# Optimization experiments

Hardware: AMD Instinct MI355X
Metric: run time of the kernel (lower is better)

Reference implementation:

```python
import jax, jax.numpy as jnp
import numpy as np

INPUT_DIM = 64
OUTPUT_DIM = 128
KNN = 10          # hardcoded min(10, N) in source
RADIUS = 0.02     # density radius in source


def setup_inputs() -> dict:
    key = jax.random.key(0)
    k1, k2, k3, k4, k5, k6, k7 = jax.random.split(key, 7)
    B, N = 2, 8192
    points = jax.random.uniform(k1, (B, N, 3), dtype=jnp.float32)
    features = jax.random.normal(k2, (B, N, INPUT_DIM), dtype=jnp.float32)
    leaf_mask = jax.random.randint(k3, (B, N), 0, 2) > 0
    d_in = INPUT_DIM + 6
    s1 = 1.0 / np.sqrt(d_in)
    s2 = 1.0 / np.sqrt(OUTPUT_DIM)
    W1 = jax.random.uniform(k4, (d_in, OUTPUT_DIM), jnp.float32, -s1, s1)
    b1 = jax.random.uniform(k5, (OUTPUT_DIM,), jnp.float32, -s1, s1)
    W2 = jax.random.uniform(k6, (OUTPUT_DIM, OUTPUT_DIM), jnp.float32, -s2, s2)
    b2 = jax.random.uniform(k7, (OUTPUT_DIM,), jnp.float32, -s2, s2)
    return {"points": points, "features": features, "leaf_mask": leaf_mask,
            "W1": W1, "b1": b1, "W2": W2, "b2": b2}


def _leaf_geometry(points, mask):
    # points: [N,3], mask: [N] bool -> [N,6]
    mask_f = mask.astype(points.dtype)
    cnt = jnp.maximum(mask_f.sum(), 1.0)
    center = (points * mask_f[:, None]).sum(0) / cnt      # mean of masked points
    rel = points - center                                  # [N,3]
    dist_c = jnp.linalg.norm(rel, axis=1)                  # dist to leaf center
    rel_h = rel[:, 2]                                      # relative height
    horiz = jnp.linalg.norm(rel[:, :2], axis=1)            # horizontal distance
    # pairwise euclidean distances [N,N]; used only for thresholding and knn
    sq = jnp.sum(points * points, axis=1)
    d2 = sq[:, None] + sq[None, :] - 2.0 * (points @ points.T)
    dist = jax.lax.stop_gradient(jnp.sqrt(jnp.maximum(d2, 0.0)))
    density = jnp.sum((dist < RADIUS) & mask[None, :], axis=1).astype(points.dtype)
    # KNN (smallest distances, includes self) -> local PCA curvature
    _, idx = jax.lax.top_k(-dist, KNN)                     # [N,KNN]
    neighbors = points[idx]                                # [N,KNN,3]
    centered = neighbors - points[:, None, :]
    cov = jnp.einsum('nki,nkj->nij', centered, centered) / float(KNN)  # [N,3,3]
    ev = jnp.linalg.eigh(cov)[0]                           # ascending eigenvalues
    curv = ev[:, 0] / (ev[:, 2] + 1e-8)
    rad = jnp.arctan2(rel[:, 1], rel[:, 0])
    geom = jnp.stack([dist_c, rel_h, horiz, density, curv, rad], axis=1)
    # source returns zeros when mask is empty
    return jnp.where(mask_f.sum() > 0, geom, jnp.zeros_like(geom))


def reference(points, features, leaf_mask, W1, b1, W2, b2):
    geom = jax.vmap(_leaf_geometry)(points, leaf_mask)     # [B,N,6]
    combined = jnp.concatenate([features, geom], axis=-1)  # [B,N,input_dim+6]
    h = jax.nn.relu(combined @ W1 + b1)
    return jax.nn.relu(h @ W2 + b2)                        # [B,N,output_dim]
```

## Files before the change

kernel.cpp:

```cpp
#include <hip/hip_runtime.h>
#include <math.h>
#include <stdint.h>

#define B_SZ   2
#define N_PTS  8192
#define IN_DIM 64
#define D_IN   70
#define ODIM   128
#define NQ_ALL (B_SZ * N_PTS)
#define RADIUS_F 0.02f

#define GDIM  32
#define NCELL (GDIM * GDIM * GDIM)
#define HCELL 0.03125f

#define SUP     4
#define NSUP_AX 8
#define NSUPER  (NSUP_AX * NSUP_AX * NSUP_AX)
#define SCAP    352
#define LCAP    24
#define MAXROWS 100

typedef unsigned long long u64;

__device__ __forceinline__ void insert11(u64 (&best)[11], u64 key) {
#pragma unroll
  for (int j = 10; j >= 1; --j) {
    u64 hi = (best[j - 1] > key) ? best[j - 1] : key;
    best[j] = (best[j] < hi) ? best[j] : hi;
  }
  best[0] = (best[0] < key) ? best[0] : key;
}
__device__ __forceinline__ void insert10(u64 (&best)[10], u64 key) {
#pragma unroll
  for (int j = 9; j >= 1; --j) {
    u64 hi = (best[j - 1] > key) ? best[j - 1] : key;
    best[j] = (best[j] < hi) ? best[j] : hi;
  }
  best[0] = (best[0] < key) ? best[0] : key;
}

__device__ __forceinline__ float sq3(float x, float y, float z) {
  return __fadd_rn(__fadd_rn(__fmul_rn(x, x), __fmul_rn(y, y)), __fmul_rn(z, z));
}

__device__ __forceinline__ int cellOf(float v) {
  int c = (int)(v * 32.0f);
  return min(max(c, 0), GDIM - 1);
}

__device__ __forceinline__ void geom_epilogue(const float* __restrict__ P,
                                              const int (&idxs)[10], float dens,
                                              float px, float py, float pz,
                                              float4 ctr, float* __restrict__ g) {
  double c00 = 0, c01 = 0, c02 = 0, c11 = 0, c12 = 0, c22 = 0;
#pragma unroll
  for (int j = 0; j < 10; ++j) {
    const int idx = idxs[j];
    const float nx = P[3 * idx + 0], ny = P[3 * idx + 1], nz = P[3 * idx + 2];
    const float ex = __fsub_rn(nx, px);
    const float ey = __fsub_rn(ny, py);
    const float ez = __fsub_rn(nz, pz);
    c00 += (double)ex * ex; c01 += (double)ex * ey; c02 += (double)ex * ez;
    c11 += (double)ey * ey; c12 += (double)ey * ez; c22 += (double)ez * ez;
  }
  const double a00 = c00 / 10.0, a01 = c01 / 10.0, a02 = c02 / 10.0;
  const double a11 = c11 / 10.0, a12 = c12 / 10.0, a22 = c22 / 10.0;

  double p1 = a01 * a01 + a02 * a02 + a12 * a12;
  double qq = (a00 + a11 + a22) / 3.0;
  double p2 = (a00 - qq) * (a00 - qq) + (a11 - qq) * (a11 - qq) +
              (a22 - qq) * (a22 - qq) + 2.0 * p1;
  double ev0, ev2;
  if (p2 <= 1e-60) {
    ev0 = ev2 = qq;
  } else {
    double p = sqrt(p2 / 6.0);
    double invp = 1.0 / p;
    double b00 = (a00 - qq) * invp, b11 = (a11 - qq) * invp, b22 = (a22 - qq) * invp;
    double b01 = a01 * invp, b02 = a02 * invp, b12 = a12 * invp;
    double detB = b00 * (b11 * b22 - b12 * b12) - b01 * (b01 * b22 - b12 * b02) +
                  b02 * (b01 * b12 - b11 * b02);
    double r = 0.5 * detB;
    r = fmin(1.0, fmax(-1.0, r));
    double phi = acos(r) / 3.0;
    ev2 = qq + 2.0 * p * cos(phi);
    ev0 = qq + 2.0 * p * cos(phi + 2.0943951023931953);
  }
  const float curv = (float)(ev0 / (ev2 + 1e-08));

  const bool on = ctr.w > 0.0f;
  const float rx = __fsub_rn(px, ctr.x);
  const float ry = __fsub_rn(py, ctr.y);
  const float rz = __fsub_rn(pz, ctr.z);
  const float dist_c = sqrtf(sq3(rx, ry, rz));
  const float horiz  = sqrtf(__fadd_rn(__fmul_rn(rx, rx), __fmul_rn(ry, ry)));
  const float rad    = atan2f(ry, rx);

  g[0] = on ? dist_c : 0.0f;
  g[1] = on ? rz : 0.0f;
  g[2] = on ? horiz : 0.0f;
  g[3] = on ? dens : 0.0f;
  g[4] = on ? curv : 0.0f;
  g[5] = on ? rad : 0.0f;
}

__global__ __launch_bounds__(256) void k_center(const float* __restrict__ points,
                                                const int* __restrict__ mask,
                                                float* __restrict__ centerOut) {
  const int b = blockIdx.x;
  const float* P = points + (size_t)b * N_PTS * 3;
  const int* M = mask + (size_t)b * N_PTS;
  double sx = 0.0, sy = 0.0, sz = 0.0, sc = 0.0;
  for (int i = threadIdx.x; i < N_PTS; i += 256) {
    if (M[i] != 0) {
      sx += (double)P[3 * i + 0];
      sy += (double)P[3 * i + 1];
      sz += (double)P[3 * i + 2];
      sc += 1.0;
    }
  }
  __shared__ double sh[4][256];
  sh[0][threadIdx.x] = sx; sh[1][threadIdx.x] = sy;
  sh[2][threadIdx.x] = sz; sh[3][threadIdx.x] = sc;
  __syncthreads();
  for (int off = 128; off > 0; off >>= 1) {
    if ((int)threadIdx.x < off) {
      sh[0][threadIdx.x] += sh[0][threadIdx.x + off];
      sh[1][threadIdx.x] += sh[1][threadIdx.x + off];
      sh[2][threadIdx.x] += sh[2][threadIdx.x + off];
      sh[3][threadIdx.x] += sh[3][threadIdx.x + off];
    }
    __syncthreads();
  }
  if (threadIdx.x == 0) {
    float cf  = (float)sh[3][0];
    float div = fmaxf(cf, 1.0f);
    centerOut[b * 4 + 0] = (float)sh[0][0] / div;
    centerOut[b * 4 + 1] = (float)sh[1][0] / div;
    centerOut[b * 4 + 2] = (float)sh[2][0] / div;
    centerOut[b * 4 + 3] = (cf > 0.0f) ? 1.0f : 0.0f;
  }
}

__global__ __launch_bounds__(256) void k_grid_count(const float* __restrict__ points,
                                                    int* __restrict__ count) {
  const int t = blockIdx.x * 256 + threadIdx.x;
  const int b = t >> 13;
  const int i = t & (N_PTS - 1);
  const float* P = points + (size_t)b * N_PTS * 3;
  const int cx = cellOf(P[3 * i + 0]);
  const int cy = cellOf(P[3 * i + 1]);
  const int cz = cellOf(P[3 * i + 2]);
  atomicAdd(&count[b * NCELL + (cz * GDIM + cy) * GDIM + cx], 1);
}

__global__ __launch_bounds__(1024) void k_scan(const int* __restrict__ count,
                                               int* __restrict__ start,
                                               int* __restrict__ cur) {
  const int b = blockIdx.x;
  const int t = threadIdx.x;
  int c[32]; int sum = 0;
#pragma unroll
  for (int j = 0; j < 32; ++j) { c[j] = count[b * NCELL + t * 32 + j]; sum += c[j]; }
  __shared__ int s[1024];
  s[t] = sum;
  __syncthreads();
  for (int off = 1; off < 1024; off <<= 1) {
    int v = (t >= off) ? s[t - off] : 0;
    __syncthreads();
    if (t >= off) s[t] += v;
    __syncthreads();
  }
  int excl = (t > 0) ? s[t - 1] : 0;
#pragma unroll
  for (int j = 0; j < 32; ++j) {
    start[b * (NCELL + 1) + t * 32 + j] = excl;
    cur[b * NCELL + t * 32 + j] = excl;
    excl += c[j];
  }
  if (t == 1023) start[b * (NCELL + 1) + NCELL] = excl;
}

__global__ __launch_bounds__(256) void k_scatter(const float* __restrict__ points,
                                                 const int* __restrict__ mask,
                                                 int* __restrict__ cur,
                                                 float4* __restrict__ sorted) {
  const int t = blockIdx.x * 256 + threadIdx.x;
  const int b = t >> 13;
  const int i = t & (N_PTS - 1);
  const float* P = points + (size_t)b * N_PTS * 3;
  const float x = P[3 * i + 0], y = P[3 * i + 1], z = P[3 * i + 2];
  const int cell = (cellOf(z) * GDIM + cellOf(y)) * GDIM + cellOf(x);
  const int pos = atomicAdd(&cur[b * NCELL + cell], 1);
  const unsigned wb = (unsigned)i | ((mask[b * N_PTS + i] != 0) ? 0x80000000u : 0u);
  sorted[(size_t)b * N_PTS + pos] = make_float4(x, y, z, __uint_as_float(wb));
}

__global__ __launch_bounds__(64) void k_collect(const float* __restrict__ points,
                                                const float4* __restrict__ sorted,
                                                const int* __restrict__ start,
                                                const float* __restrict__ center,
                                                float* __restrict__ geom,
                                                int* __restrict__ list,
                                                int* __restrict__ listCnt,
                                                float COLLECT_T, float DENS_T,
                                                float THR_CHECK) {
  const int b  = blockIdx.y;
  const int sc = blockIdx.x;
  const int sx = sc & 7, sy = (sc >> 3) & 7, sz = sc >> 6;
  const int lane = threadIdx.x;

  const int* ST = start + b * (NCELL + 1);
  const float4* SP = sorted + (size_t)b * N_PTS;

  const int x0 = SUP * sx, x1 = SUP * sx + SUP - 1;
  const int y0 = SUP * sy, y1 = SUP * sy + SUP - 1;
  const int z0 = SUP * sz, z1 = SUP * sz + SUP - 1;
  const int hx0 = max(x0 - 3, 0), hx1 = min(x1 + 3, GDIM - 1);
  const int hy0 = max(y0 - 3, 0), hy1 = min(y1 + 3, GDIM - 1);
  const int hz0 = max(z0 - 3, 0), hz1 = min(z1 + 3, GDIM - 1);
  const int yc = hy1 - hy0 + 1;
  const int R  = (hz1 - hz0 + 1) * yc;

  __shared__ int    rs[MAXROWS], rp[MAXROWS + 1];
  __shared__ int    qs_[16], qp_[17];
  __shared__ float4 pts4[SCAP];
  __shared__ u64    lbuf[64 * LCAP];

  {
    int qlen = 0, qst = 0;
    if (lane < 16) {
      const int z = z0 + (lane >> 2), y = y0 + (lane & 3);
      const int base = (z * GDIM + y) * GDIM;
      qst  = ST[base + x0];
      qlen = ST[base + x1 + 1] - qst;
    }
    int inc = qlen;
    for (int off = 1; off < 64; off <<= 1) { int v = __shfl_up(inc, off); if (lane >= off) inc += v; }
    if (lane < 16) { qs_[lane] = qst; qp_[lane] = inc - qlen; }
    if (lane == 63) qp_[16] = inc;
  }
  {
    int len[2] = {0, 0}, st2[2] = {0, 0};
#pragma unroll
    for (int k = 0; k < 2; ++k) {
      const int r = lane * 2 + k;
      if (r < R) {
        const int z = hz0 + r / yc, y = hy0 + r % yc;
        const int base = (z * GDIM + y) * GDIM;
        st2[k] = ST[base + hx0];
        len[k] = ST[base + hx1 + 1] - st2[k];
      }
    }
    int sum = len[0] + len[1];
    int inc = sum;
    for (int off = 1; off < 64; off <<= 1) { int v = __shfl_up(inc, off); if (lane >= off) inc += v; }
    int exc = inc - sum;
#pragma unroll
    for (int k = 0; k < 2; ++k) {
      const int r = lane * 2 + k;
      if (r < R) { rs[r] = st2[k]; rp[r] = exc; }
      exc += len[k];
    }
    if (lane == 63) rp[R] = inc;
  }
  __syncthreads();

  const int C    = rp[R];
  const int qtot = qp_[16];
  if (qtot == 0) return;

  if (C > SCAP) {
    for (int t = lane; t < qtot; t += 64) {
      int lo = 0, hi = 15;
      while (lo < hi) { const int mid = (lo + hi + 1) >> 1; if (qp_[mid] <= t) lo = mid; else hi = mid - 1; }
      const int qglob = qs_[lo] + (t - qp_[lo]);
      const int pos = atomicAdd(listCnt, 1);
      list[pos] = (b << 13) | qglob;
    }
    return;
  }

  for (int i = lane; i < C; i += 64) {
    int lo = 0, hi = R - 1;
    while (lo < hi) { const int mid = (lo + hi + 1) >> 1; if (rp[mid] <= i) lo = mid; else hi = mid - 1; }
    pts4[i] = SP[rs[lo] + (i - rp[lo])];
  }
  __syncthreads();

  const float4 ctr = reinterpret_cast<const float4*>(center)[b];
  const float* P = points + (size_t)b * N_PTS * 3;
  const int sub = lane & 3;
  const int gq  = lane >> 2;

  for (int q0 = 0; q0 < qtot; q0 += 16) {
    const int myq = q0 + gq;
    const bool act = (myq < qtot);
    const int mq = act ? myq : 0;
    int lo = 0, hi = 15;
    while (lo < hi) { const int mid = (lo + hi + 1) >> 1; if (qp_[mid] <= mq) lo = mid; else hi = mid - 1; }
    const int qglob = qs_[lo] + (mq - qp_[lo]);
    const float4 qp4 = SP[qglob];
    const int qidx = (int)(__float_as_uint(qp4.w) & 0x7FFFFFFFu);
    const float px = qp4.x, py = qp4.y, pz = qp4.z;
    const float sqq = sq3(px, py, pz);

    int cnt = 0;
    u64* myb = &lbuf[lane * LCAP];
    for (int j = sub; j < C; j += 4) {
      const float4 tp = pts4[j];
      const float sqc = sq3(tp.x, tp.y, tp.z);
      const float dot = __fmaf_rn(pz, tp.z, __fmaf_rn(py, tp.y, __fmul_rn(px, tp.x)));
      const float d2  = __fsub_rn(__fadd_rn(sqq, sqc), __fmul_rn(2.0f, dot));
      const float d2c = fmaxf(d2, 0.0f);
      if (d2c < COLLECT_T) {
        if (cnt < LCAP) {
          const unsigned wb = __float_as_uint(tp.w);
          myb[cnt] = ((u64)__float_as_uint(d2c) << 32)
                   | (u64)(((wb & 0x7FFFFFFFu) << 1) | (wb >> 31));
        }
        ++cnt;
      }
    }

    u64 best[11];
#pragma unroll
    for (int j = 0; j < 11; ++j) best[j] = ~0ull;
    float dens = 0.0f;
    const int m = min(cnt, LCAP);
    for (int i = 0; i < m; ++i) {
      const u64 e = myb[i];
      if ((e & 1ull) && __uint_as_float((unsigned)(e >> 32)) < DENS_T) dens += 1.0f;
      if (e < best[10]) insert11(best, e);
    }
    int cntg = cnt;
    int over = (cnt > LCAP) ? 1 : 0;
#pragma unroll
    for (int s = 1; s < 4; s <<= 1) {
      dens += __shfl_xor(dens, s);
      cntg += __shfl_xor(cntg, s);
      over |= __shfl_xor(over, s);
      u64 ok[11];
#pragma unroll
      for (int j = 0; j < 11; ++j) ok[j] = __shfl_xor(best[j], s);
#pragma unroll
      for (int j = 0; j < 11; ++j) {
        if (ok[j] < best[10]) insert11(best, ok[j]); else break;
      }
    }

    if (act && sub == 0) {
      const float dist9 = sqrtf(__uint_as_float((unsigned)(best[9] >> 32)));
      bool bad = (over != 0) || (cntg < 10) || !(dist9 < THR_CHECK);
      if (cntg >= 11) {
        const float dist10 = sqrtf(__uint_as_float((unsigned)(best[10] >> 32)));
        bad = bad || (dist10 == dist9);
      }
      if (bad) {
        const int pos = atomicAdd(listCnt, 1);
        list[pos] = (b << 13) | qglob;
      } else {
        int idxs[10];
#pragma unroll
        for (int j = 0; j < 10; ++j) idxs[j] = (int)(((unsigned)best[j]) >> 1);
        geom_epilogue(P, idxs, dens, px, py, pz, ctr,
                      geom + ((size_t)b * N_PTS + qidx) * 6);
      }
    }
  }
}

__global__ __launch_bounds__(64) void k_wavefb(const float* __restrict__ points,
                                               const float4* __restrict__ sorted,
                                               const int* __restrict__ start,
                                               const float* __restrict__ center,
                                               float* __restrict__ geom,
                                               int* __restrict__ flags2,
                                               const int* __restrict__ list,
                                               const int* __restrict__ listCnt) {
  const int lane = threadIdx.x;
  const int n = *listCnt;
  for (int it = blockIdx.x; it < n; it += gridDim.x) {
    const int e = list[it];
    const int b = e >> 13, qs = e & (N_PTS - 1);
    const float4* SP = sorted + (size_t)b * N_PTS;
    const int* ST = start + b * (NCELL + 1);
    const float4 qp = SP[qs];
    const int qidx = (int)(__float_as_uint(qp.w) & 0x7FFFFFFFu);
    const float px = qp.x, py = qp.y, pz = qp.z;
    const float sqq = sq3(px, py, pz);
    const int cx = cellOf(px), cy = cellOf(py), cz = cellOf(pz);
    const int xlo = max(cx - 8, 0), xhi = min(cx + 8, GDIM - 1);
    const int ylo = max(cy - 8, 0), yhi = min(cy + 8, GDIM - 1);
    const int zlo = max(cz - 8, 0), zhi = min(cz + 8, GDIM - 1);
    const int ycw = yhi - ylo + 1;
    const int Rw = (zhi - zlo + 1) * ycw;

    u64 best[10];
#pragma unroll
    for (int j = 0; j < 10; ++j) best[j] = ((u64)0x7F800000u << 32) | 0xFFFFFFFFu;
    float dens = 0.0f;

    for (int r = lane; r < Rw; r += 64) {
      const int z = zlo + r / ycw, y = ylo + r % ycw;
      const int base = (z * GDIM + y) * GDIM;
      const int j0 = ST[base + xlo], j1 = ST[base + xhi + 1];
      for (int j = j0; j < j1; ++j) {
        const float4 tp = SP[j];
        const unsigned wb = __float_as_uint(tp.w);
        const float sqc = sq3(tp.x, tp.y, tp.z);
        const float dot = __fmaf_rn(pz, tp.z, __fmaf_rn(py, tp.y, __fmul_rn(px, tp.x)));
        const float d2  = __fsub_rn(__fadd_rn(sqq, sqc), __fmul_rn(2.0f, dot));
        const float dist = sqrtf(fmaxf(d2, 0.0f));
        if ((dist < RADIUS_F) && (wb & 0x80000000u)) dens += 1.0f;
        const u64 key = ((u64)__float_as_uint(dist) << 32) | (wb & 0x7FFFFFFFu);
        if (key < best[9]) insert10(best, key);
      }
    }
#pragma unroll
    for (int s = 1; s < 64; s <<= 1) {
      dens += __shfl_xor(dens, s);
      u64 ok[10];
#pragma unroll
      for (int j = 0; j < 10; ++j) ok[j] = __shfl_xor(best[j], s);
#pragma unroll
      for (int j = 0; j < 10; ++j) {
        if (ok[j] < best[9]) insert10(best, ok[j]); else break;
      }
    }
    if (lane == 0) {
      const float dist9 = __uint_as_float((unsigned)(best[9] >> 32));
      if (dist9 < 0.2494f) {
        const float4 ctr = reinterpret_cast<const float4*>(center)[b];
        const float* P = points + (size_t)b * N_PTS * 3;
        int idxs[10];
#pragma unroll
        for (int j = 0; j < 10; ++j) idxs[j] = (int)(((unsigned)best[j]) & 0x7FFFFFFFu);
        geom_epilogue(P, idxs, dens, px, py, pz, ctr, geom + ((size_t)b * N_PTS + qidx) * 6);
      } else {
        flags2[b * N_PTS + qs] = 1;
      }
    }
  }
}

__global__ __launch_bounds__(256) void k_fallback(const float* __restrict__ points,
                                                  const float4* __restrict__ sorted,
                                                  const int* __restrict__ start,
                                                  const float* __restrict__ center,
                                                  float* __restrict__ geom,
                                                  const int* __restrict__ flags2) {
  const int b = blockIdx.y;
  const int qs = blockIdx.x * 256 + threadIdx.x;
  if (flags2[b * N_PTS + qs] == 0) return;
  const float4 qp = sorted[(size_t)b * N_PTS + qs];
  const unsigned qw = __float_as_uint(qp.w);
  const int qidx = (int)(qw & 0x7FFFFFFFu);

  const float px = qp.x, py = qp.y, pz = qp.z;
  const float sqq = sq3(px, py, pz);
  const int cx = cellOf(px), cy = cellOf(py), cz = cellOf(pz);

  const int* ST = start + b * (NCELL + 1);
  const float4* SP = sorted + (size_t)b * N_PTS;

  u64 best[10];
#pragma unroll
  for (int j = 0; j < 10; ++j) best[j] = ((u64)0x7F800000u << 32) | 0xFFFFFFFFu;
  float dens = 0.0f;

  for (int rho = 0; rho < GDIM; ++rho) {
    const int zlo = max(cz - rho, 0), zhi = min(cz + rho, GDIM - 1);
    const int ylo = max(cy - rho, 0), yhi = min(cy + rho, GDIM - 1);
    for (int z = zlo; z <= zhi; ++z) {
      const int adz = abs(z - cz);
      for (int y = ylo; y <= yhi; ++y) {
        const int ady = abs(y - cy);
        const int m2 = max(adz, ady);
        int ja, jb;
        int ja2 = 0, jb2 = 0;
        const int rowBase = (z * GDIM + y) * GDIM;
        if (m2 == rho) {
          const int xa = max(cx - rho, 0), xb = min(cx + rho, GDIM - 1);
          ja = ST[rowBase + xa]; jb = ST[rowBase + xb + 1];
        } else {
          ja = jb = 0;
          if (cx - rho >= 0)        { ja = ST[rowBase + cx - rho]; jb = ST[rowBase + cx - rho + 1]; }
          if (cx + rho <= GDIM - 1) { ja2 = ST[rowBase + cx + rho]; jb2 = ST[rowBase + cx + rho + 1]; }
        }
#pragma unroll 1
        for (int pass = 0; pass < 2; ++pass) {
          const int j0 = pass ? ja2 : ja;
          const int j1 = pass ? jb2 : jb;
          for (int j = j0; j < j1; ++j) {
            const float4 tp = SP[j];
            const unsigned wb = __float_as_uint(tp.w);
            const float sqc = sq3(tp.x, tp.y, tp.z);
            const float dot = __fmaf_rn(pz, tp.z, __fmaf_rn(py, tp.y, __fmul_rn(px, tp.x)));
            const float d2  = __fsub_rn(__fadd_rn(sqq, sqc), __fmul_rn(2.0f, dot));
            const float dist = sqrtf(fmaxf(d2, 0.0f));
            if ((dist < RADIUS_F) && (wb & 0x80000000u)) dens += 1.0f;
            const u64 key = ((u64)__float_as_uint(dist) << 32) | (wb & 0x7FFFFFFFu);
            if (key < best[9]) insert10(best, key);
          }
        }
      }
    }
    if (rho >= 1) {
      const float dist9 = __uint_as_float((unsigned)(best[9] >> 32));
      if (dist9 < (float)rho * HCELL * 0.999f) break;
    }
  }

  const float4 ctr = reinterpret_cast<const float4*>(center)[b];
  const float* P = points + (size_t)b * N_PTS * 3;
  int idxs[10];
#pragma unroll
  for (int j = 0; j < 10; ++j) idxs[j] = (int)(((unsigned)best[j]) & 0x7FFFFFFFu);
  geom_epilogue(P, idxs, dens, px, py, pz, ctr, geom + ((size_t)b * N_PTS + qidx) * 6);
}

__global__ __launch_bounds__(256) void k_mlp(const float* __restrict__ features,
                                             const float* __restrict__ geom,
                                             const float* __restrict__ W1,
                                             const float* __restrict__ b1,
                                             const float* __restrict__ W2,
                                             const float* __restrict__ b2,
                                             float* __restrict__ out) {
  __shared__ float A[64][74];
  __shared__ float H[64][130];
  const int tid = threadIdx.x;
  const int row0 = blockIdx.x * 64;

  for (int i = tid; i < 64 * IN_DIM; i += 256) {
    int r = i >> 6, k = i & 63;
    A[r][k] = features[(size_t)(row0 + r) * IN_DIM + k];
  }
  for (int i = tid; i < 64 * 8; i += 256) {
    int r = i >> 3, k = i & 7;
    if (k < 6) A[r][IN_DIM + k] = geom[(size_t)(row0 + r) * 6 + k];
  }
  __syncthreads();

  const int ty = tid >> 4;
  const int tx = tid & 15;

  float acc[4][8];
#pragma unroll
  for (int i = 0; i < 4; ++i)
#pragma unroll
    for (int j = 0; j < 8; ++j) acc[i][j] = 0.0f;

#pragma unroll 2
  for (int k = 0; k < D_IN; ++k) {
    float a[4];
#pragma unroll
    for (int i = 0; i < 4; ++i) a[i] = A[ty * 4 + i][k];
    float4 w0 = *reinterpret_cast<const float4*>(&W1[(size_t)k * ODIM + tx * 8]);
    float4 w1 = *reinterpret_cast<const float4*>(&W1[(size_t)k * ODIM + tx * 8 + 4]);
    float w[8] = {w0.x, w0.y, w0.z, w0.w, w1.x, w1.y, w1.z, w1.w};
#pragma unroll
    for (int i = 0; i < 4; ++i)
#pragma unroll
      for (int j = 0; j < 8; ++j) acc[i][j] = fmaf(a[i], w[j], acc[i][j]);
  }

  {
    float4 bb0 = *reinterpret_cast<const float4*>(&b1[tx * 8]);
    float4 bb1 = *reinterpret_cast<const float4*>(&b1[tx * 8 + 4]);
    float bb[8] = {bb0.x, bb0.y, bb0.z, bb0.w, bb1.x, bb1.y, bb1.z, bb1.w};
#pragma unroll
    for (int i = 0; i < 4; ++i) {
      float4 h0 = make_float4(fmaxf(acc[i][0] + bb[0], 0.f), fmaxf(acc[i][1] + bb[1], 0.f),
                              fmaxf(acc[i][2] + bb[2], 0.f), fmaxf(acc[i][3] + bb[3], 0.f));
      float4 h1 = make_float4(fmaxf(acc[i][4] + bb[4], 0.f), fmaxf(acc[i][5] + bb[5], 0.f),
                              fmaxf(acc[i][6] + bb[6], 0.f), fmaxf(acc[i][7] + bb[7], 0.f));
      *reinterpret_cast<float4*>(&H[ty * 4 + i][tx * 8]) = h0;
      *reinterpret_cast<float4*>(&H[ty * 4 + i][tx * 8 + 4]) = h1;
    }
  }
  __syncthreads();

#pragma unroll
  for (int i = 0; i < 4; ++i)
#pragma unroll
    for (int j = 0; j < 8; ++j) acc[i][j] = 0.0f;

#pragma unroll 2
  for (int k = 0; k < ODIM; ++k) {
    float a[4];
#pragma unroll
    for (int i = 0; i < 4; ++i) a[i] = H[ty * 4 + i][k];
    float4 w0 = *reinterpret_cast<const float4*>(&W2[(size_t)k * ODIM + tx * 8]);
    float4 w1 = *reinterpret_cast<const float4*>(&W2[(size_t)k * ODIM + tx * 8 + 4]);
    float w[8] = {w0.x, w0.y, w0.z, w0.w, w1.x, w1.y, w1.z, w1.w};
#pragma unroll
    for (int i = 0; i < 4; ++i)
#pragma unroll
      for (int j = 0; j < 8; ++j) acc[i][j] = fmaf(a[i], w[j], acc[i][j]);
  }

  {
    float4 bb0 = *reinterpret_cast<const float4*>(&b2[tx * 8]);
    float4 bb1 = *reinterpret_cast<const float4*>(&b2[tx * 8 + 4]);
    float bb[8] = {bb0.x, bb0.y, bb0.z, bb0.w, bb1.x, bb1.y, bb1.z, bb1.w};
#pragma unroll
    for (int i = 0; i < 4; ++i) {
      size_t row = (size_t)(row0 + ty * 4 + i);
      float4 o0 = make_float4(fmaxf(acc[i][0] + bb[0], 0.f), fmaxf(acc[i][1] + bb[1], 0.f),
                              fmaxf(acc[i][2] + bb[2], 0.f), fmaxf(acc[i][3] + bb[3], 0.f));
      float4 o1 = make_float4(fmaxf(acc[i][4] + bb[4], 0.f), fmaxf(acc[i][5] + bb[5], 0.f),
                              fmaxf(acc[i][6] + bb[6], 0.f), fmaxf(acc[i][7] + bb[7], 0.f));
      *reinterpret_cast<float4*>(&out[row * ODIM + tx * 8]) = o0;
      *reinterpret_cast<float4*>(&out[row * ODIM + tx * 8 + 4]) = o1;
    }
  }
}

extern "C" void kernel_launch(void* const* d_in, const int* in_sizes, int n_in,
                              void* d_out, int out_size, void* d_ws, size_t ws_size,
                              hipStream_t stream) {
  const float* points   = (const float*)d_in[0];
  const float* features = (const float*)d_in[1];
  const int*   mask     = (const int*)d_in[2];
  const float* W1       = (const float*)d_in[3];
  const float* b1       = (const float*)d_in[4];
  const float* W2       = (const float*)d_in[5];
  const float* b2       = (const float*)d_in[6];
  float* out = (float*)d_out;

  const double Rd   = (double)0.02f;
  const double midd = Rd - ldexp(1.0, -30);
  const double Td   = midd * midd;
  float densT = (float)Td;
  if ((double)densT <= Td) densT = nextafterf(densT, 1.0f);
  const float collectT = 0.0935f * 0.0935f;
  const float thrCheck = 0.0934f;

  char* w = (char*)d_ws;
  size_t off = 0;
  auto take = [&](size_t bytes) { char* p = w + off; off = (off + bytes + 255) & ~(size_t)255; return p; };
  float*  geomBuf   = (float*)take((size_t)NQ_ALL * 6 * 4);
  float*  centerBuf = (float*)take(2 * 16);
  char*   zero0     = (char*)take(0);
  int*    countBuf  = (int*)take((size_t)B_SZ * NCELL * 4);
  int*    flags2Buf = (int*)take((size_t)NQ_ALL * 4);
  int*    listCnt   = (int*)take(4);
  char*   zero1     = (char*)take(0);
  int*    startBuf  = (int*)take((size_t)B_SZ * (NCELL + 1) * 4);
  int*    curBuf    = (int*)take((size_t)B_SZ * NCELL * 4);
  float4* sortedBuf = (float4*)take((size_t)B_SZ * N_PTS * 16);
  int*    listBuf   = (int*)take((size_t)NQ_ALL * 4);
  (void)ws_size;

  hipMemsetAsync(zero0, 0, (size_t)(zero1 - zero0), stream);
  k_center<<<B_SZ, 256, 0, stream>>>(points, mask, centerBuf);
  k_grid_count<<<NQ_ALL / 256, 256, 0, stream>>>(points, countBuf);
  k_scan<<<B_SZ, 1024, 0, stream>>>(countBuf, startBuf, curBuf);
  k_scatter<<<NQ_ALL / 256, 256, 0, stream>>>(points, mask, curBuf, sortedBuf);
  k_collect<<<dim3(NSUPER, B_SZ), 64, 0, stream>>>(points, sortedBuf, startBuf, centerBuf,
                                                   geomBuf, listBuf, listCnt,
                                                   collectT, densT, thrCheck);
  k_wavefb<<<1024, 64, 0, stream>>>(points, sortedBuf, startBuf, centerBuf,
                                    geomBuf, flags2Buf, listBuf, listCnt);
  k_fallback<<<dim3(N_PTS / 256, B_SZ), 256, 0, stream>>>(points, sortedBuf, startBuf,
                                                          centerBuf, geomBuf, flags2Buf);
  k_mlp<<<NQ_ALL / 64, 256, 0, stream>>>(features, geomBuf, W1, b1, W2, b2, out);
}
```

Baseline: 227.2 us.

## Fuse center reduction into grid count, widen collect blocks, shrink MLP row tiles

Folds the mask-center reduction into the grid-count kernel, using wave shuffles and double atomics, and finalizes the center inside the scan kernel, which removes a two-block serial launch. The collect kernel goes from 64 to 128 threads per block, handling 32 queries per pass with a 2x unrolled candidate loop. The MLP uses 32-row tiles so twice as many blocks run with fewer accumulators per thread. Double atomics make the center sum order nondeterministic, and the larger collect blocks use more LDS per block.

```diff
diff --git a/kernel.cpp b/kernel.cpp
--- a/kernel.cpp
+++ b/kernel.cpp
@@ -20,6 +20,8 @@
 #define SCAP    352
 #define LCAP    24
 #define MAXROWS 100
+
+#define MROWS   32
 
 typedef unsigned long long u64;
 
@@ -105,61 +107,52 @@
   g[5] = on ? rad : 0.0f;
 }
 
-__global__ __launch_bounds__(256) void k_center(const float* __restrict__ points,
-                                                const int* __restrict__ mask,
-                                                float* __restrict__ centerOut) {
-  const int b = blockIdx.x;
-  const float* P = points + (size_t)b * N_PTS * 3;
-  const int* M = mask + (size_t)b * N_PTS;
-  double sx = 0.0, sy = 0.0, sz = 0.0, sc = 0.0;
-  for (int i = threadIdx.x; i < N_PTS; i += 256) {
-    if (M[i] != 0) {
-      sx += (double)P[3 * i + 0];
-      sy += (double)P[3 * i + 1];
-      sz += (double)P[3 * i + 2];
-      sc += 1.0;
-    }
-  }
-  __shared__ double sh[4][256];
-  sh[0][threadIdx.x] = sx; sh[1][threadIdx.x] = sy;
-  sh[2][threadIdx.x] = sz; sh[3][threadIdx.x] = sc;
-  __syncthreads();
-  for (int off = 128; off > 0; off >>= 1) {
-    if ((int)threadIdx.x < off) {
-      sh[0][threadIdx.x] += sh[0][threadIdx.x + off];
-      sh[1][threadIdx.x] += sh[1][threadIdx.x + off];
-      sh[2][threadIdx.x] += sh[2][threadIdx.x + off];
-      sh[3][threadIdx.x] += sh[3][threadIdx.x + off];
-    }
-    __syncthreads();
-  }
-  if (threadIdx.x == 0) {
-    float cf  = (float)sh[3][0];
-    float div = fmaxf(cf, 1.0f);
-    centerOut[b * 4 + 0] = (float)sh[0][0] / div;
-    centerOut[b * 4 + 1] = (float)sh[1][0] / div;
-    centerOut[b * 4 + 2] = (float)sh[2][0] / div;
-    centerOut[b * 4 + 3] = (cf > 0.0f) ? 1.0f : 0.0f;
-  }
-}
-
-__global__ __launch_bounds__(256) void k_grid_count(const float* __restrict__ points,
-                                                    int* __restrict__ count) {
+__global__ __launch_bounds__(256) void k_build(const float* __restrict__ points,
+                                               const int* __restrict__ mask,
+                                               int* __restrict__ count,
+                                               double* __restrict__ ctrAcc) {
   const int t = blockIdx.x * 256 + threadIdx.x;
   const int b = t >> 13;
   const int i = t & (N_PTS - 1);
   const float* P = points + (size_t)b * N_PTS * 3;
-  const int cx = cellOf(P[3 * i + 0]);
-  const int cy = cellOf(P[3 * i + 1]);
-  const int cz = cellOf(P[3 * i + 2]);
-  atomicAdd(&count[b * NCELL + (cz * GDIM + cy) * GDIM + cx], 1);
+  const float x = P[3 * i + 0], y = P[3 * i + 1], z = P[3 * i + 2];
+  atomicAdd(&count[b * NCELL + (cellOf(z) * GDIM + cellOf(y)) * GDIM + cellOf(x)], 1);
+
+  const bool m = mask[b * N_PTS + i] != 0;
+  double vx = m ? (double)x : 0.0, vy = m ? (double)y : 0.0;
+  double vz = m ? (double)z : 0.0, vc = m ? 1.0 : 0.0;
+#pragma unroll
+  for (int s = 1; s < 64; s <<= 1) {
+    vx += __shfl_xor(vx, s); vy += __shfl_xor(vy, s);
+    vz += __shfl_xor(vz, s); vc += __shfl_xor(vc, s);
+  }
+  __shared__ double sh[4][4];
+  const int w = threadIdx.x >> 6;
+  if ((threadIdx.x & 63) == 0) { sh[0][w] = vx; sh[1][w] = vy; sh[2][w] = vz; sh[3][w] = vc; }
+  __syncthreads();
+  if (threadIdx.x == 0) {
+    atomicAdd(&ctrAcc[b * 4 + 0], sh[0][0] + sh[0][1] + sh[0][2] + sh[0][3]);
+    atomicAdd(&ctrAcc[b * 4 + 1], sh[1][0] + sh[1][1] + sh[1][2] + sh[1][3]);
+    atomicAdd(&ctrAcc[b * 4 + 2], sh[2][0] + sh[2][1] + sh[2][2] + sh[2][3]);
+    atomicAdd(&ctrAcc[b * 4 + 3], sh[3][0] + sh[3][1] + sh[3][2] + sh[3][3]);
+  }
 }
 
 __global__ __launch_bounds__(1024) void k_scan(const int* __restrict__ count,
                                                int* __restrict__ start,
-                                               int* __restrict__ cur) {
+                                               int* __restrict__ cur,
+                                               const double* __restrict__ ctrAcc,
+                                               float* __restrict__ centerOut) {
   const int b = blockIdx.x;
   const int t = threadIdx.x;
+  if (t == 0) {
+    const float cf = (float)ctrAcc[b * 4 + 3];
+    const float div = fmaxf(cf, 1.0f);
+    centerOut[b * 4 + 0] = (float)ctrAcc[b * 4 + 0] / div;
+    centerOut[b * 4 + 1] = (float)ctrAcc[b * 4 + 1] / div;
+    centerOut[b * 4 + 2] = (float)ctrAcc[b * 4 + 2] / div;
+    centerOut[b * 4 + 3] = (cf > 0.0f) ? 1.0f : 0.0f;
+  }
   int c[32]; int sum = 0;
 #pragma unroll
   for (int j = 0; j < 32; ++j) { c[j] = count[b * NCELL + t * 32 + j]; sum += c[j]; }
@@ -197,19 +190,19 @@
   sorted[(size_t)b * N_PTS + pos] = make_float4(x, y, z, __uint_as_float(wb));
 }
 
-__global__ __launch_bounds__(64) void k_collect(const float* __restrict__ points,
-                                                const float4* __restrict__ sorted,
-                                                const int* __restrict__ start,
-                                                const float* __restrict__ center,
-                                                float* __restrict__ geom,
-                                                int* __restrict__ list,
-                                                int* __restrict__ listCnt,
-                                                float COLLECT_T, float DENS_T,
-                                                float THR_CHECK) {
+__global__ __launch_bounds__(128) void k_collect(const float* __restrict__ points,
+                                                 const float4* __restrict__ sorted,
+                                                 const int* __restrict__ start,
+                                                 const float* __restrict__ center,
+                                                 float* __restrict__ geom,
+                                                 int* __restrict__ list,
+                                                 int* __restrict__ listCnt,
+                                                 float COLLECT_T, float DENS_T,
+                                                 float THR_CHECK) {
   const int b  = blockIdx.y;
   const int sc = blockIdx.x;
   const int sx = sc & 7, sy = (sc >> 3) & 7, sz = sc >> 6;
-  const int lane = threadIdx.x;
+  const int tid = threadIdx.x;
 
   const int* ST = start + b * (NCELL + 1);
   const float4* SP = sorted + (size_t)b * N_PTS;
@@ -226,44 +219,46 @@
   __shared__ int    rs[MAXROWS], rp[MAXROWS + 1];
   __shared__ int    qs_[16], qp_[17];
   __shared__ float4 pts4[SCAP];
-  __shared__ u64    lbuf[64 * LCAP];
-
-  {
-    int qlen = 0, qst = 0;
-    if (lane < 16) {
-      const int z = z0 + (lane >> 2), y = y0 + (lane & 3);
-      const int base = (z * GDIM + y) * GDIM;
-      qst  = ST[base + x0];
-      qlen = ST[base + x1 + 1] - qst;
-    }
-    int inc = qlen;
-    for (int off = 1; off < 64; off <<= 1) { int v = __shfl_up(inc, off); if (lane >= off) inc += v; }
-    if (lane < 16) { qs_[lane] = qst; qp_[lane] = inc - qlen; }
-    if (lane == 63) qp_[16] = inc;
-  }
-  {
-    int len[2] = {0, 0}, st2[2] = {0, 0};
-#pragma unroll
-    for (int k = 0; k < 2; ++k) {
-      const int r = lane * 2 + k;
-      if (r < R) {
-        const int z = hz0 + r / yc, y = hy0 + r % yc;
+  __shared__ u64    lbuf[128 * LCAP];
+
+  if (tid < 64) {
+    {
+      int qlen = 0, qst = 0;
+      if (tid < 16) {
+        const int z = z0 + (tid >> 2), y = y0 + (tid & 3);
         const int base = (z * GDIM + y) * GDIM;
-        st2[k] = ST[base + hx0];
-        len[k] = ST[base + hx1 + 1] - st2[k];
-      }
-    }
-    int sum = len[0] + len[1];
-    int inc = sum;
-    for (int off = 1; off < 64; off <<= 1) { int v = __shfl_up(inc, off); if (lane >= off) inc += v; }
-    int exc = inc - sum;
-#pragma unroll
-    for (int k = 0; k < 2; ++k) {
-      const int r = lane * 2 + k;
-      if (r < R) { rs[r] = st2[k]; rp[r] = exc; }
-      exc += len[k];
-    }
-    if (lane == 63) rp[R] = inc;
+        qst  = ST[base + x0];
+        qlen = ST[base + x1 + 1] - qst;
+      }
+      int inc = qlen;
+      for (int off = 1; off < 64; off <<= 1) { int v = __shfl_up(inc, off); if (tid >= off) inc += v; }
+      if (tid < 16) { qs_[tid] = qst; qp_[tid] = inc - qlen; }
+      if (tid == 63) qp_[16] = inc;
+    }
+    {
+      int len[2] = {0, 0}, st2[2] = {0, 0};
+#pragma unroll
+      for (int k = 0; k < 2; ++k) {
+        const int r = tid * 2 + k;
+        if (r < R) {
+          const int z = hz0 + r / yc, y = hy0 + r % yc;
+          const int base = (z * GDIM + y) * GDIM;
+          st2[k] = ST[base + hx0];
+          len[k] = ST[base + hx1 + 1] - st2[k];
+        }
+      }
+      int sum = len[0] + len[1];
+      int inc = sum;
+      for (int off = 1; off < 64; off <<= 1) { int v = __shfl_up(inc, off); if (tid >= off) inc += v; }
+      int exc = inc - sum;
+#pragma unroll
+      for (int k = 0; k < 2; ++k) {
+        const int r = tid * 2 + k;
+        if (r < R) { rs[r] = st2[k]; rp[r] = exc; }
+        exc += len[k];
+      }
+      if (tid == 63) rp[R] = inc;
+    }
   }
   __syncthreads();
 
@@ -272,7 +267,7 @@
   if (qtot == 0) return;
 
   if (C > SCAP) {
-    for (int t = lane; t < qtot; t += 64) {
+    for (int t = tid; t < qtot; t += 128) {
       int lo = 0, hi = 15;
       while (lo < hi) { const int mid = (lo + hi + 1) >> 1; if (qp_[mid] <= t) lo = mid; else hi = mid - 1; }
       const int qglob = qs_[lo] + (t - qp_[lo]);
@@ -282,7 +277,7 @@
     return;
   }
 
-  for (int i = lane; i < C; i += 64) {
+  for (int i = tid; i < C; i += 128) {
     int lo = 0, hi = R - 1;
     while (lo < hi) { const int mid = (lo + hi + 1) >> 1; if (rp[mid] <= i) lo = mid; else hi = mid - 1; }
     pts4[i] = SP[rs[lo] + (i - rp[lo])];
@@ -291,10 +286,10 @@
 
   const float4 ctr = reinterpret_cast<const float4*>(center)[b];
   const float* P = points + (size_t)b * N_PTS * 3;
-  const int sub = lane & 3;
-  const int gq  = lane >> 2;
-
-  for (int q0 = 0; q0 < qtot; q0 += 16) {
+  const int sub = tid & 3;
+  const int gq  = tid >> 2;
+
+  for (int q0 = 0; q0 < qtot; q0 += 32) {
     const int myq = q0 + gq;
     const bool act = (myq < qtot);
     const int mq = act ? myq : 0;
@@ -307,7 +302,8 @@
     const float sqq = sq3(px, py, pz);
 
     int cnt = 0;
-    u64* myb = &lbuf[lane * LCAP];
+    u64* myb = &lbuf[tid * LCAP];
+#pragma unroll 2
     for (int j = sub; j < C; j += 4) {
       const float4 tp = pts4[j];
       const float sqc = sq3(tp.x, tp.y, tp.z);
@@ -528,92 +524,91 @@
                                              const float* __restrict__ W2,
                                              const float* __restrict__ b2,
                                              float* __restrict__ out) {
-  __shared__ float A[64][74];
-  __shared__ float H[64][130];
+  __shared__ float A[MROWS][71];
+  __shared__ float H[MROWS][133];
   const int tid = threadIdx.x;
-  const int row0 = blockIdx.x * 64;
-
-  for (int i = tid; i < 64 * IN_DIM; i += 256) {
+  const int row0 = blockIdx.x * MROWS;
+
+  for (int i = tid; i < MROWS * IN_DIM; i += 256) {
     int r = i >> 6, k = i & 63;
     A[r][k] = features[(size_t)(row0 + r) * IN_DIM + k];
   }
-  for (int i = tid; i < 64 * 8; i += 256) {
+  for (int i = tid; i < MROWS * 8; i += 256) {
     int r = i >> 3, k = i & 7;
     if (k < 6) A[r][IN_DIM + k] = geom[(size_t)(row0 + r) * 6 + k];
   }
   __syncthreads();
 
-  const int ty = tid >> 4;
-  const int tx = tid & 15;
-
-  float acc[4][8];
-#pragma unroll
-  for (int i = 0; i < 4; ++i)
+  const int r0 = tid >> 4;
+  const int c  = (tid & 15) * 8;
+
+  float acc[2][8];
+#pragma unroll
+  for (int i = 0; i < 2; ++i)
 #pragma unroll
     for (int j = 0; j < 8; ++j) acc[i][j] = 0.0f;
 
 #pragma unroll 2
   for (int k = 0; k < D_IN; ++k) {
-    float a[4];
-#pragma unroll
-    for (int i = 0; i < 4; ++i) a[i] = A[ty * 4 + i][k];
-    float4 w0 = *reinterpret_cast<const float4*>(&W1[(size_t)k * ODIM + tx * 8]);
-    float4 w1 = *reinterpret_cast<const float4*>(&W1[(size_t)k * ODIM + tx * 8 + 4]);
-    float w[8] = {w0.x, w0.y, w0.z, w0.w, w1.x, w1.y, w1.z, w1.w};
-#pragma unroll
-    for (int i = 0; i < 4; ++i)
-#pragma unroll
-      for (int j = 0; j < 8; ++j) acc[i][j] = fmaf(a[i], w[j], acc[i][j]);
-  }
-
+    const float a0 = A[r0][k];
+    const float a1 = A[r0 + 16][k];
+    const float4 w0 = *reinterpret_cast<const float4*>(&W1[(size_t)k * ODIM + c]);
+    const float4 w1 = *reinterpret_cast<const float4*>(&W1[(size_t)k * ODIM + c + 4]);
+    const float w[8] = {w0.x, w0.y, w0.z, w0.w, w1.x, w1.y, w1.z, w1.w};
+#pragma unroll
+    for (int j = 0; j < 8; ++j) {
+      acc[0][j] = fmaf(a0, w[j], acc[0][j]);
+      acc[1][j] = fmaf(a1, w[j], acc[1][j]);
+    }
+  }
   {
-    float4 bb0 = *reinterpret_cast<const float4*>(&b1[tx * 8]);
-    float4 bb1 = *reinterpret_cast<const float4*>(&b1[tx * 8 + 4]);
-    float bb[8] = {bb0.x, bb0.y, bb0.z, bb0.w, bb1.x, bb1.y, bb1.z, bb1.w};
-#pragma unroll
-    for (int i = 0; i < 4; ++i) {
+    const float4 bb0 = *reinterpret_cast<const float4*>(&b1[c]);
+    const float4 bb1 = *reinterpret_cast<const float4*>(&b1[c + 4]);
+    const float bb[8] = {bb0.x, bb0.y, bb0.z, bb0.w, bb1.x, bb1.y, bb1.z, bb1.w};
+#pragma unroll
+    for (int i = 0; i < 2; ++i) {
+      const int rr = r0 + 16 * i;
       float4 h0 = make_float4(fmaxf(acc[i][0] + bb[0], 0.f), fmaxf(acc[i][1] + bb[1], 0.f),
                               fmaxf(acc[i][2] + bb[2], 0.f), fmaxf(acc[i][3] + bb[3], 0.f));
       float4 h1 = make_float4(fmaxf(acc[i][4] + bb[4], 0.f), fmaxf(acc[i][5] + bb[5], 0.f),
                               fmaxf(acc[i][6] + bb[6], 0.f), fmaxf(acc[i][7] + bb[7], 0.f));
-      *reinterpret_cast<float4*>(&H[ty * 4 + i][tx * 8]) = h0;
-      *reinterpret_cast<float4*>(&H[ty * 4 + i][tx * 8 + 4]) = h1;
+      *reinterpret_cast<float4*>(&H[rr][c]) = h0;
+      *reinterpret_cast<float4*>(&H[rr][c + 4]) = h1;
     }
   }
   __syncthreads();
 
 #pragma unroll
-  for (int i = 0; i < 4; ++i)
+  for (int i = 0; i < 2; ++i)
 #pragma unroll
     for (int j = 0; j < 8; ++j) acc[i][j] = 0.0f;
 
 #pragma unroll 2
   for (int k = 0; k < ODIM; ++k) {
-    float a[4];
-#pragma unroll
-    for (int i = 0; i < 4; ++i) a[i] = H[ty * 4 + i][k];
-    float4 w0 = *reinterpret_cast<const float4*>(&W2[(size_t)k * ODIM + tx * 8]);
-    float4 w1 = *reinterpret_cast<const float4*>(&W2[(size_t)k * ODIM + tx * 8 + 4]);
-    float w[8] = {w0.x, w0.y, w0.z, w0.w, w1.x, w1.y, w1.z, w1.w};
-#pragma unroll
-    for (int i = 0; i < 4; ++i)
-#pragma unroll
-      for (int j = 0; j < 8; ++j) acc[i][j] = fmaf(a[i], w[j], acc[i][j]);
-  }
-
+    const float a0 = H[r0][k];
+    const float a1 = H[r0 + 16][k];
+    const float4 w0 = *reinterpret_cast<const float4*>(&W2[(size_t)k * ODIM + c]);
+    const float4 w1 = *reinterpret_cast<const float4*>(&W2[(size_t)k * ODIM + c + 4]);
+    const float w[8] = {w0.x, w0.y, w0.z, w0.w, w1.x, w1.y, w1.z, w1.w};
+#pragma unroll
+    for (int j = 0; j < 8; ++j) {
+      acc[0][j] = fmaf(a0, w[j], acc[0][j]);
+      acc[1][j] = fmaf(a1, w[j], acc[1][j]);
+    }
+  }
   {
-    float4 bb0 = *reinterpret_cast<const float4*>(&b2[tx * 8]);
-    float4 bb1 = *reinterpret_cast<const float4*>(&b2[tx * 8 + 4]);
-    float bb[8] = {bb0.x, bb0.y, bb0.z, bb0.w, bb1.x, bb1.y, bb1.z, bb1.w};
-#pragma unroll
-    for (int i = 0; i < 4; ++i) {
-      size_t row = (size_t)(row0 + ty * 4 + i);
+    const float4 bb0 = *reinterpret_cast<const float4*>(&b2[c]);
+    const float4 bb1 = *reinterpret_cast<const float4*>(&b2[c + 4]);
+    const float bb[8] = {bb0.x, bb0.y, bb0.z, bb0.w, bb1.x, bb1.y, bb1.z, bb1.w};
+#pragma unroll
+    for (int i = 0; i < 2; ++i) {
+      const size_t row = (size_t)(row0 + r0 + 16 * i);
       float4 o0 = make_float4(fmaxf(acc[i][0] + bb[0], 0.f), fmaxf(acc[i][1] + bb[1], 0.f),
                               fmaxf(acc[i][2] + bb[2], 0.f), fmaxf(acc[i][3] + bb[3], 0.f));
       float4 o1 = make_float4(fmaxf(acc[i][4] + bb[4], 0.f), fmaxf(acc[i][5] + bb[5], 0.f),
                               fmaxf(acc[i][6] + bb[6], 0.f), fmaxf(acc[i][7] + bb[7], 0.f));
-      *reinterpret_cast<float4*>(&out[row * ODIM + tx * 8]) = o0;
-      *reinterpret_cast<float4*>(&out[row * ODIM + tx * 8 + 4]) = o1;
+      *reinterpret_cast<float4*>(&out[row * ODIM + c]) = o0;
+      *reinterpret_cast<float4*>(&out[row * ODIM + c + 4]) = o1;
     }
   }
 }
@@ -647,6 +642,7 @@
   int*    countBuf  = (int*)take((size_t)B_SZ * NCELL * 4);
   int*    flags2Buf = (int*)take((size_t)NQ_ALL * 4);
   int*    listCnt   = (int*)take(4);
+  double* ctrAcc    = (double*)take((size_t)B_SZ * 4 * 8);
   char*   zero1     = (char*)take(0);
   int*    startBuf  = (int*)take((size_t)B_SZ * (NCELL + 1) * 4);
   int*    curBuf    = (int*)take((size_t)B_SZ * NCELL * 4);
@@ -655,16 +651,15 @@
   (void)ws_size;
 
   hipMemsetAsync(zero0, 0, (size_t)(zero1 - zero0), stream);
-  k_center<<<B_SZ, 256, 0, stream>>>(points, mask, centerBuf);
-  k_grid_count<<<NQ_ALL / 256, 256, 0, stream>>>(points, countBuf);
-  k_scan<<<B_SZ, 1024, 0, stream>>>(countBuf, startBuf, curBuf);
+  k_build<<<NQ_ALL / 256, 256, 0, stream>>>(points, mask, countBuf, ctrAcc);
+  k_scan<<<B_SZ, 1024, 0, stream>>>(countBuf, startBuf, curBuf, ctrAcc, centerBuf);
   k_scatter<<<NQ_ALL / 256, 256, 0, stream>>>(points, mask, curBuf, sortedBuf);
-  k_collect<<<dim3(NSUPER, B_SZ), 64, 0, stream>>>(points, sortedBuf, startBuf, centerBuf,
-                                                   geomBuf, listBuf, listCnt,
-                                                   collectT, densT, thrCheck);
+  k_collect<<<dim3(NSUPER, B_SZ), 128, 0, stream>>>(points, sortedBuf, startBuf, centerBuf,
+                                                    geomBuf, listBuf, listCnt,
+                                                    collectT, densT, thrCheck);
   k_wavefb<<<1024, 64, 0, stream>>>(points, sortedBuf, startBuf, centerBuf,
                                     geomBuf, flags2Buf, listBuf, listCnt);
   k_fallback<<<dim3(N_PTS / 256, B_SZ), 256, 0, stream>>>(points, sortedBuf, startBuf,
                                                           centerBuf, geomBuf, flags2Buf);
-  k_mlp<<<NQ_ALL / 64, 256, 0, stream>>>(features, geomBuf, W1, b1, W2, b2, out);
-}
+  k_mlp<<<NQ_ALL / MROWS, 256, 0, stream>>>(features, geomBuf, W1, b1, W2, b2, out);
+}
```

Measured after the change: 186.5 us. -17.9%, faster.
